# Kernel optimization log

Measured on AMD Instinct MI355X. Metric: run time of the kernel, lower is better.

## Reference

```python
import jax, jax.numpy as jnp
import numpy as np

B, D, T = 16, 512, 2048
H = 2
HD = D // H

def setup_inputs() -> dict:
    key = jax.random.key(0)
    k1, k2, k3, k4 = jax.random.split(key, 4)
    s_in = 1.0 / np.sqrt(D)   # torch default-like uniform init for weight_matrix
    s_t = 1.0 / np.sqrt(T)    # nn.Linear default init bound
    xs = jax.random.normal(k1, (B, D, T), dtype=jnp.float32)
    W_KQ = jax.random.uniform(k2, (D, D), jnp.float32, -s_in, s_in)
    W_PV = jax.random.uniform(k3, (D, D), jnp.float32, -s_in, s_in)
    W_out = jax.random.uniform(k4, (T, T), jnp.float32, -s_t, s_t)
    return {"xs": xs, "W_KQ": W_KQ, "W_PV": W_PV, "W_out": W_out}

def reference(xs, W_KQ, W_PV, W_out):
    b, d, t = xs.shape
    xs_skip = xs[:, :, :-1]                                   # [B, D, T-1]
    # xskq = xs_skip^T @ W_KQ  -> [B, T-1, D]
    xskq = jnp.einsum('bds,dj->bsj', xs_skip, W_KQ)
    # split heads: [B, H, T-1, HD]
    xskq_split = xskq.reshape(b, t - 1, H, HD).transpose(0, 2, 1, 3)
    # xs reshaped to heads along feature dim: [B, H, HD, T]
    xs_r = xs.reshape(b, H, HD, t)
    attn_arg = jnp.matmul(xskq_split, xs_r)                   # [B, H, T-1, T], rho=1
    # NON-STANDARD: softmax over the head axis (size 2)
    sm = jax.nn.softmax(attn_arg, axis=1)
    # W_PV @ xs_skip -> [B, D, T-1], split into heads [B, H, HD, T-1]
    wpvx = jnp.einsum('id,bds->bis', W_PV, xs_skip).reshape(b, H, HD, t - 1)
    f_attn = jnp.matmul(wpvx, sm).reshape(b, d, t)            # [B, D, T]
    # output = Linear(T, T, bias=None) then take last token:
    # out[b, i] = sum_t f_attn[b, i, t] * W_out[T-1, t]
    out = jnp.einsum('bdt,t->bd', f_attn, W_out[-1])
    return out
```

## Files before the change

### kernel.cpp

```cpp
#include <hip/hip_runtime.h>
#include <hip/hip_bf16.h>

#define NB 16
#define ND 512
#define NT 2048
#define TM1 2047
#define NHD 256

typedef __attribute__((ext_vector_type(8))) short bf16x8;
typedef __attribute__((ext_vector_type(4))) float f32x4;
typedef unsigned short ushort_t;
typedef unsigned int uint_t;

#define G0_OFF    0ull
#define G0_ELEMS  (16ull * 2047ull)
#define R0_OFF    32768ull
#define SX_OFF    40960ull
#define ZERO_FLOATS 49152ull
#define WSUM_OFF  49152ull
#define WKQT_OFF  49408ull
#define CHUNK_OFF 180480ull
#define BATCH_US  (2048ull * 512ull)
#define BATCH_FLOATS (2ull * 524288ull)

__device__ __forceinline__ ushort_t f2bf(float x) {
    union { float f; uint_t u; } v; v.f = x;
    uint_t r = v.u + 0x7FFFu + ((v.u >> 16) & 1u);
    return (ushort_t)(r >> 16);
}
__device__ __forceinline__ float bf2f(uint_t u) {
    union { uint_t u; float f; } v; v.u = u << 16;
    return v.f;
}

__device__ __forceinline__ void async_copy16(const ushort_t* g, ushort_t* l) {
    __builtin_amdgcn_global_load_lds(
        (const __attribute__((address_space(1))) void*)g,
        (__attribute__((address_space(3))) void*)l, 16, 0, 0);
}

#define FENCE() asm volatile("" ::: "memory")
#define BARRIER() do { FENCE(); __builtin_amdgcn_s_barrier(); FENCE(); } while (0)
#define WAITVM4() asm volatile("s_waitcnt vmcnt(4)" ::: "memory")
#define WAITVM0() asm volatile("s_waitcnt vmcnt(0)" ::: "memory")

__global__ __launch_bounds__(256) void k_prep(const float* __restrict__ wkq,
                                              ushort_t* __restrict__ wkqT,
                                              const float* __restrict__ wlast,
                                              float* __restrict__ wsum,
                                              float* __restrict__ zbase) {
    __shared__ float tile[32][33];
    const int j0 = blockIdx.x * 32, d0 = blockIdx.y * 32;
    const int c = threadIdx.x & 31, r = threadIdx.x >> 5;
    #pragma unroll
    for (int i = 0; i < 4; ++i) {
        const int d = r + i * 8;
        tile[d][c] = wkq[(size_t)(d0 + d) * ND + j0 + c];
    }
    __syncthreads();
    #pragma unroll
    for (int i = 0; i < 4; ++i) {
        const int j = r + i * 8;
        wkqT[(size_t)(j0 + j) * ND + d0 + c] = f2bf(tile[c][j]);
    }
    const int bid = blockIdx.y * 16 + blockIdx.x;
    if (threadIdx.x < 192) zbase[bid * 192 + threadIdx.x] = 0.f;
    if (bid == 0) {
        __shared__ float red[256];
        float s = 0.f;
        for (int t = threadIdx.x; t < NT; t += 256) s += wlast[t];
        red[threadIdx.x] = s;
        __syncthreads();
        for (int off = 128; off > 0; off >>= 1) {
            if (threadIdx.x < off) red[threadIdx.x] += red[threadIdx.x + off];
            __syncthreads();
        }
        if (threadIdx.x == 0) *wsum = red[0];
    }
}

__global__ __launch_bounds__(256) void k_cvt_xst(const float* __restrict__ xs,
                                                 ushort_t* __restrict__ xst, int b0) {
    __shared__ float tile[64][257];
    const int t0 = blockIdx.x * 256, d0 = blockIdx.y * 64;
    const int cc = blockIdx.z;
    const float* xb = xs + (size_t)(b0 + cc) * ND * NT;
    ushort_t* xo = xst + (size_t)cc * BATCH_US;
    const int wave = threadIdx.x >> 6, lane = threadIdx.x & 63;
    #pragma unroll
    for (int i = 0; i < 16; ++i) {
        const int row = wave * 16 + i;
        *(float4*)&tile[row][lane * 4] =
            *(const float4*)&xb[(size_t)(d0 + row) * NT + t0 + lane * 4];
    }
    __syncthreads();
    const int c8 = (threadIdx.x & 7) * 8;
    #pragma unroll
    for (int i = 0; i < 8; ++i) {
        const int t = i * 32 + (threadIdx.x >> 3);
        uint_t w[4];
        #pragma unroll
        for (int p = 0; p < 4; ++p)
            w[p] = (uint_t)f2bf(tile[c8 + 2 * p][t]) |
                   ((uint_t)f2bf(tile[c8 + 2 * p + 1][t]) << 16);
        *(uint4*)&xo[(size_t)(t0 + t) * ND + d0 + c8] = *(uint4*)w;
    }
}

__global__ __launch_bounds__(256) void k_qd(const ushort_t* __restrict__ xst,
                                            const ushort_t* __restrict__ wkqT,
                                            ushort_t* __restrict__ qdb) {
    const int j0 = blockIdx.x * 128;
    const int s0 = blockIdx.y * 128;
    const int cc = blockIdx.z;
    __shared__ __align__(16) ushort_t As[128 * 64];
    __shared__ __align__(16) ushort_t Bs[128 * 64];
    const int tid = threadIdx.x;
    const int wave = tid >> 6, lane = tid & 63;
    const int l15 = lane & 15, quad = lane >> 4;
    const int wm = wave >> 1, wn = wave & 1;
    const int swz = l15 & 7;
    const int lrow = lane >> 3;
    const size_t lsrc = (size_t)lrow * ND + (size_t)(((lane & 7) ^ lrow) << 3);
    const ushort_t* xa = xst + (size_t)cc * BATCH_US + (size_t)s0 * ND;
    const ushort_t* wb = wkqT + (size_t)j0 * ND;
    ushort_t* qo = qdb + (size_t)cc * BATCH_US;
    f32x4 acc[4][4];
    #pragma unroll
    for (int mi = 0; mi < 4; ++mi)
        #pragma unroll
        for (int nj = 0; nj < 4; ++nj) acc[mi][nj] = (f32x4){0.f, 0.f, 0.f, 0.f};
    for (int ks = 0; ks < 8; ++ks) {
        const int k0 = ks * 64;
        #pragma unroll
        for (int n = 0; n < 4; ++n) {
            const int rbase = wave * 32 + n * 8;
            async_copy16(xa + (size_t)rbase * ND + k0 + lsrc, &As[rbase * 64]);
            async_copy16(wb + (size_t)rbase * ND + k0 + lsrc, &Bs[rbase * 64]);
        }
        __builtin_amdgcn_s_waitcnt(0);
        __syncthreads();
        #pragma unroll
        for (int kc = 0; kc < 2; ++kc) {
            bf16x8 af[4], bfr[4];
            #pragma unroll
            for (int mi = 0; mi < 4; ++mi)
                af[mi] = *(const bf16x8*)&As[(wm * 64 + mi * 16 + l15) * 64 + (((kc * 4 + quad) ^ swz) << 3)];
            #pragma unroll
            for (int nj = 0; nj < 4; ++nj)
                bfr[nj] = *(const bf16x8*)&Bs[(wn * 64 + nj * 16 + l15) * 64 + (((kc * 4 + quad) ^ swz) << 3)];
            #pragma unroll
            for (int mi = 0; mi < 4; ++mi)
                #pragma unroll
                for (int nj = 0; nj < 4; ++nj)
                    acc[mi][nj] = __builtin_amdgcn_mfma_f32_16x16x32_bf16(af[mi], bfr[nj], acc[mi][nj], 0, 0, 0);
        }
        __syncthreads();
    }
    #pragma unroll
    for (int mi = 0; mi < 4; ++mi) {
        const int srow = s0 + wm * 64 + mi * 16 + quad * 4;
        #pragma unroll
        for (int nj = 0; nj < 4; ++nj) {
            const int jcol = j0 + wn * 64 + nj * 16 + l15;
            const float sgn = (jcol < NHD) ? 1.f : -1.f;
            #pragma unroll
            for (int r = 0; r < 4; ++r)
                qo[(size_t)(srow + r) * ND + jcol] = f2bf(sgn * acc[mi][nj][r]);
        }
    }
}

__device__ __forceinline__ void ld_frag4(bf16x8 (&dst)[4][2], const ushort_t* buf,
                                         int rbase, int l15, int quad, int swz) {
    #pragma unroll
    for (int i = 0; i < 4; ++i)
        #pragma unroll
        for (int kc = 0; kc < 2; ++kc)
            dst[i][kc] = *(const bf16x8*)&buf[(rbase + i * 16 + l15) * 64 + (((kc * 4 + quad) ^ swz) << 3)];
}
__device__ __forceinline__ void ld_frag2(bf16x8 (&dst)[2][2], const ushort_t* buf,
                                         int rbase, int l15, int quad, int swz) {
    #pragma unroll
    for (int i = 0; i < 2; ++i)
        #pragma unroll
        for (int kc = 0; kc < 2; ++kc)
            dst[i][kc] = *(const bf16x8*)&buf[(rbase + i * 16 + l15) * 64 + (((kc * 4 + quad) ^ swz) << 3)];
}
__device__ __forceinline__ void mfma8(f32x4 (&acc)[8][4], const bf16x8 (&a)[4][2],
                                      const bf16x8 (&bb)[2][2], int mbase, int nbase) {
    __builtin_amdgcn_s_setprio(1);
    #pragma unroll
    for (int kc = 0; kc < 2; ++kc)
        #pragma unroll
        for (int mi = 0; mi < 4; ++mi)
            #pragma unroll
            for (int nj = 0; nj < 2; ++nj)
                acc[mbase + mi][nbase + nj] = __builtin_amdgcn_mfma_f32_16x16x32_bf16(
                    a[mi][kc], bb[nj][kc], acc[mbase + mi][nbase + nj], 0, 0, 0);
    __builtin_amdgcn_s_setprio(0);
}

__global__ __launch_bounds__(512, 2) void k_attn(const ushort_t* __restrict__ qdb,
                                                 const ushort_t* __restrict__ xst,
                                                 const float* __restrict__ wlast,
                                                 float* __restrict__ g0, int b0) {
    const int t0 = blockIdx.x * 256;
    const int s0 = blockIdx.y * 256;
    const int cc = blockIdx.z;
    const int b = b0 + cc;
    __shared__ __align__(16) ushort_t smA[2][16384];
    __shared__ __align__(16) ushort_t smB[2][16384];
    __shared__ float lds_g[256];
    const int tid = threadIdx.x;
    const int wave = tid >> 6, lane = tid & 63;
    const int l15 = lane & 15, quad = lane >> 4;
    const int wm = wave >> 2, wn = wave & 3;
    const int swz = l15 & 7;
    const int lrow = lane >> 3;
    const size_t lsrc = (size_t)lrow * ND + (size_t)(((lane & 7) ^ lrow) << 3);
    const ushort_t* Ag = qdb + (size_t)cc * BATCH_US + (size_t)s0 * ND;
    const ushort_t* Bg = xst + (size_t)cc * BATCH_US + (size_t)t0 * ND;

#define STAGE(gb_, buf_, kt_, h_) do {                                        \
        const ushort_t* g_ = (gb_) + (size_t)((h_) * 128 + wave * 8) * ND +   \
                             (kt_) * 64 + lsrc;                               \
        ushort_t* l_ = (buf_) + (h_) * 8192 + wave * 512;                     \
        async_copy16(g_, l_);                                                 \
        async_copy16(g_ + (size_t)64 * ND, l_ + 4096);                        \
    } while (0)

    f32x4 acc[8][4];
    #pragma unroll
    for (int mi = 0; mi < 8; ++mi)
        #pragma unroll
        for (int nj = 0; nj < 4; ++nj) acc[mi][nj] = (f32x4){0.f, 0.f, 0.f, 0.f};
    bf16x8 a[4][2], br[2][2][2];

    STAGE(Bg, smB[0], 0, 0); STAGE(Bg, smB[0], 0, 1);
    STAGE(Ag, smA[0], 0, 0); STAGE(Ag, smA[0], 0, 1);
    STAGE(Bg, smB[1], 1, 0); STAGE(Bg, smB[1], 1, 1);
    WAITVM4();
    BARRIER();

    #pragma unroll
    for (int j = 0; j < 4; ++j) {
        const int kO = 2 * j + 1;
        ld_frag4(a, smA[0], wm * 128, l15, quad, swz);
        ld_frag2(br[0], smB[0], wn * 64, l15, quad, swz);
        STAGE(Ag, smA[1], kO, 0);
        BARRIER();
        mfma8(acc, a, br[0], 0, 0);
        BARRIER();
        ld_frag2(br[1], smB[0], wn * 64 + 32, l15, quad, swz);
        STAGE(Ag, smA[1], kO, 1);
        BARRIER();
        mfma8(acc, a, br[1], 0, 2);
        BARRIER();
        ld_frag4(a, smA[0], wm * 128 + 64, l15, quad, swz);
        if (j < 3) STAGE(Bg, smB[0], 2 * j + 2, 0);
        BARRIER();
        mfma8(acc, a, br[0], 4, 0);
        BARRIER();
        if (j < 3) STAGE(Bg, smB[0], 2 * j + 2, 1);
        BARRIER();
        mfma8(acc, a, br[1], 4, 2);
        if (j < 3) { WAITVM4(); } else { WAITVM0(); }
        BARRIER();
        ld_frag4(a, smA[1], wm * 128, l15, quad, swz);
        ld_frag2(br[0], smB[1], wn * 64, l15, quad, swz);
        if (j < 3) STAGE(Ag, smA[0], 2 * j + 2, 0);
        BARRIER();
        mfma8(acc, a, br[0], 0, 0);
        BARRIER();
        ld_frag2(br[1], smB[1], wn * 64 + 32, l15, quad, swz);
        if (j < 3) STAGE(Ag, smA[0], 2 * j + 2, 1);
        BARRIER();
        mfma8(acc, a, br[1], 0, 2);
        BARRIER();
        ld_frag4(a, smA[1], wm * 128 + 64, l15, quad, swz);
        if (j < 3) STAGE(Bg, smB[1], kO + 2, 0);
        BARRIER();
        mfma8(acc, a, br[0], 4, 0);
        BARRIER();
        if (j < 3) STAGE(Bg, smB[1], kO + 2, 1);
        BARRIER();
        mfma8(acc, a, br[1], 4, 2);
        if (j < 3) WAITVM4();
        BARRIER();
    }
#undef STAGE

    if (tid < 256) lds_g[tid] = 0.f;
    __syncthreads();
    float wt[4];
    #pragma unroll
    for (int nj = 0; nj < 4; ++nj) wt[nj] = wlast[t0 + wn * 64 + nj * 16 + l15];
    #pragma unroll
    for (int mi = 0; mi < 8; ++mi) {
        #pragma unroll
        for (int r = 0; r < 4; ++r) {
            float v = 0.f;
            #pragma unroll
            for (int nj = 0; nj < 4; ++nj) {
                const float e = __expf(-acc[mi][nj][r]);
                v = fmaf(__builtin_amdgcn_rcpf(1.f + e), wt[nj], v);
            }
            v += __shfl_xor(v, 1);
            v += __shfl_xor(v, 2);
            v += __shfl_xor(v, 4);
            v += __shfl_xor(v, 8);
            if (l15 == 0) atomicAdd(&lds_g[wm * 128 + mi * 16 + quad * 4 + r], v);
        }
    }
    __syncthreads();
    if (tid < 256) {
        const int srow = s0 + tid;
        if (srow < TM1) atomicAdd(&g0[b * TM1 + srow], lds_g[tid]);
    }
}

__global__ __launch_bounds__(256) void k_r(const ushort_t* __restrict__ xst,
                                           const float* __restrict__ g0,
                                           float* __restrict__ r0acc,
                                           float* __restrict__ sxacc, int b0) {
    const int sc = blockIdx.x;
    const int cc = blockIdx.y;
    const int b = b0 + cc;
    const ushort_t* xa = xst + (size_t)cc * BATCH_US;
    const float* g = g0 + b * TM1;
    const int d2 = threadIdx.x;
    float a00 = 0.f, a01 = 0.f, a10 = 0.f, a11 = 0.f;
    const int send = (sc == 31) ? 63 : 64;
    for (int si = 0; si < send; ++si) {
        const int s = sc * 64 + si;
        const float gv = g[s];
        const uint_t pk = *(const uint_t*)&xa[(size_t)s * ND + d2 * 2];
        const float x0 = bf2f(pk & 0xFFFFu);
        const float x1 = bf2f(pk >> 16);
        a00 = fmaf(x0, gv, a00); a01 = fmaf(x1, gv, a01);
        a10 += x0; a11 += x1;
    }
    atomicAdd(&r0acc[b * ND + d2 * 2], a00);
    atomicAdd(&r0acc[b * ND + d2 * 2 + 1], a01);
    atomicAdd(&sxacc[b * ND + d2 * 2], a10);
    atomicAdd(&sxacc[b * ND + d2 * 2 + 1], a11);
}

__global__ __launch_bounds__(256) void k_out(const float* __restrict__ wpv,
                                             const float* __restrict__ r0acc,
                                             const float* __restrict__ sxacc,
                                             const float* __restrict__ wsum,
                                             float* __restrict__ out) {
    const int b = blockIdx.x;
    const int i0 = blockIdx.y * 256;
    __shared__ float rs[1024];
    const float wsv = *wsum;
    for (int i = threadIdx.x; i < ND; i += 256) {
        const float r0 = r0acc[b * ND + i];
        const float sx = sxacc[b * ND + i];
        rs[i] = r0;
        rs[ND + i] = fmaf(wsv, sx, -r0);
    }
    __syncthreads();
    const int i = i0 + threadIdx.x;
    const float* wrow = wpv + (size_t)i * ND;
    const float* rh = rs + (i >> 8) * ND;
    float acc = 0.f;
    for (int dd = 0; dd < ND; dd += 4) {
        const float4 wv = *(const float4*)(wrow + dd);
        acc += wv.x * rh[dd] + wv.y * rh[dd + 1] + wv.z * rh[dd + 2] + wv.w * rh[dd + 3];
    }
    out[b * ND + i] = acc;
}

extern "C" void kernel_launch(void* const* d_in, const int* in_sizes, int n_in,
                              void* d_out, int out_size, void* d_ws, size_t ws_size,
                              hipStream_t stream) {
    (void)in_sizes; (void)n_in; (void)out_size;
    const float* xs   = (const float*)d_in[0];
    const float* wkq  = (const float*)d_in[1];
    const float* wpv  = (const float*)d_in[2];
    const float* wout = (const float*)d_in[3];
    const float* wlast = wout + (size_t)(NT - 1) * NT;

    float* ws    = (float*)d_ws;
    float* g0    = ws + G0_OFF;
    float* r0acc = ws + R0_OFF;
    float* sxacc = ws + SX_OFF;
    float* wsum  = ws + WSUM_OFF;
    ushort_t* wkqT = (ushort_t*)(ws + WKQT_OFF);

    const size_t ws_floats = ws_size / 4;
    size_t avail = (ws_floats > CHUNK_OFF) ? (ws_floats - CHUNK_OFF) : 0;
    int C = (int)(avail / BATCH_FLOATS);
    if (C > NB) C = NB;
    if (C < 1) C = 1;
    ushort_t* qdb = (ushort_t*)(ws + CHUNK_OFF);
    ushort_t* xst = (ushort_t*)(ws + CHUNK_OFF + (size_t)C * 524288ull);

    k_prep<<<dim3(16, 16), 256, 0, stream>>>(wkq, wkqT, wlast, wsum, ws);
    for (int b0 = 0; b0 < NB; b0 += C) {
        const int cb = (NB - b0 < C) ? (NB - b0) : C;
        k_cvt_xst<<<dim3(8, 8, cb), 256, 0, stream>>>(xs, xst, b0);
        k_qd     <<<dim3(4, 16, cb),  256, 0, stream>>>(xst, wkqT, qdb);
        k_attn   <<<dim3(8, 8, cb),  512, 0, stream>>>(qdb, xst, wlast, g0, b0);
        k_r      <<<dim3(32, cb),     256, 0, stream>>>(xst, g0, r0acc, sxacc, b0);
    }
    k_out<<<dim3(NB, 2), 256, 0, stream>>>(wpv, r0acc, sxacc, wsum, (float*)d_out);
}
```

Measured before the change: 275.0 us.

## Reuse pipelined 256x256 GEMM core for QD projection and remap workgroups for XCD locality

Factors the 8-phase double-buffered MFMA GEMM from k_attn into a shared device function and rewrites k_qd to use it with 256x256 tiles and 512 threads, replacing the simple 128x128 single-buffered loop. Both k_qd and k_attn now remap the linear block id so that consecutive logical tiles land on the same XCD (round-robin over 8), aiming to improve L2 reuse of shared operand rows. The cost is fewer, larger blocks for k_qd (256 per batch chunk fewer in count), which may reduce occupancy and balance; the XCD remap assumes the grid size is divisible by 8.

```diff
diff --git a/kernel.cpp b/kernel.cpp
--- a/kernel.cpp
+++ b/kernel.cpp
@@ -107,70 +107,6 @@
     }
 }
 
-__global__ __launch_bounds__(256) void k_qd(const ushort_t* __restrict__ xst,
-                                            const ushort_t* __restrict__ wkqT,
-                                            ushort_t* __restrict__ qdb) {
-    const int j0 = blockIdx.x * 128;
-    const int s0 = blockIdx.y * 128;
-    const int cc = blockIdx.z;
-    __shared__ __align__(16) ushort_t As[128 * 64];
-    __shared__ __align__(16) ushort_t Bs[128 * 64];
-    const int tid = threadIdx.x;
-    const int wave = tid >> 6, lane = tid & 63;
-    const int l15 = lane & 15, quad = lane >> 4;
-    const int wm = wave >> 1, wn = wave & 1;
-    const int swz = l15 & 7;
-    const int lrow = lane >> 3;
-    const size_t lsrc = (size_t)lrow * ND + (size_t)(((lane & 7) ^ lrow) << 3);
-    const ushort_t* xa = xst + (size_t)cc * BATCH_US + (size_t)s0 * ND;
-    const ushort_t* wb = wkqT + (size_t)j0 * ND;
-    ushort_t* qo = qdb + (size_t)cc * BATCH_US;
-    f32x4 acc[4][4];
-    #pragma unroll
-    for (int mi = 0; mi < 4; ++mi)
-        #pragma unroll
-        for (int nj = 0; nj < 4; ++nj) acc[mi][nj] = (f32x4){0.f, 0.f, 0.f, 0.f};
-    for (int ks = 0; ks < 8; ++ks) {
-        const int k0 = ks * 64;
-        #pragma unroll
-        for (int n = 0; n < 4; ++n) {
-            const int rbase = wave * 32 + n * 8;
-            async_copy16(xa + (size_t)rbase * ND + k0 + lsrc, &As[rbase * 64]);
-            async_copy16(wb + (size_t)rbase * ND + k0 + lsrc, &Bs[rbase * 64]);
-        }
-        __builtin_amdgcn_s_waitcnt(0);
-        __syncthreads();
-        #pragma unroll
-        for (int kc = 0; kc < 2; ++kc) {
-            bf16x8 af[4], bfr[4];
-            #pragma unroll
-            for (int mi = 0; mi < 4; ++mi)
-                af[mi] = *(const bf16x8*)&As[(wm * 64 + mi * 16 + l15) * 64 + (((kc * 4 + quad) ^ swz) << 3)];
-            #pragma unroll
-            for (int nj = 0; nj < 4; ++nj)
-                bfr[nj] = *(const bf16x8*)&Bs[(wn * 64 + nj * 16 + l15) * 64 + (((kc * 4 + quad) ^ swz) << 3)];
-            #pragma unroll
-            for (int mi = 0; mi < 4; ++mi)
-                #pragma unroll
-                for (int nj = 0; nj < 4; ++nj)
-                    acc[mi][nj] = __builtin_amdgcn_mfma_f32_16x16x32_bf16(af[mi], bfr[nj], acc[mi][nj], 0, 0, 0);
-        }
-        __syncthreads();
-    }
-    #pragma unroll
-    for (int mi = 0; mi < 4; ++mi) {
-        const int srow = s0 + wm * 64 + mi * 16 + quad * 4;
-        #pragma unroll
-        for (int nj = 0; nj < 4; ++nj) {
-            const int jcol = j0 + wn * 64 + nj * 16 + l15;
-            const float sgn = (jcol < NHD) ? 1.f : -1.f;
-            #pragma unroll
-            for (int r = 0; r < 4; ++r)
-                qo[(size_t)(srow + r) * ND + jcol] = f2bf(sgn * acc[mi][nj][r]);
-        }
-    }
-}
-
 __device__ __forceinline__ void ld_frag4(bf16x8 (&dst)[4][2], const ushort_t* buf,
                                          int rbase, int l15, int quad, int swz) {
     #pragma unroll
@@ -201,26 +137,20 @@
     __builtin_amdgcn_s_setprio(0);
 }
 
-__global__ __launch_bounds__(512, 2) void k_attn(const ushort_t* __restrict__ qdb,
-                                                 const ushort_t* __restrict__ xst,
-                                                 const float* __restrict__ wlast,
-                                                 float* __restrict__ g0, int b0) {
-    const int t0 = blockIdx.x * 256;
-    const int s0 = blockIdx.y * 256;
-    const int cc = blockIdx.z;
-    const int b = b0 + cc;
-    __shared__ __align__(16) ushort_t smA[2][16384];
-    __shared__ __align__(16) ushort_t smB[2][16384];
-    __shared__ float lds_g[256];
+__device__ __forceinline__ void gemm8ph(const ushort_t* __restrict__ Ag,
+                                        const ushort_t* __restrict__ Bg,
+                                        ushort_t* __restrict__ smA0, ushort_t* __restrict__ smA1,
+                                        ushort_t* __restrict__ smB0, ushort_t* __restrict__ smB1,
+                                        f32x4 (&acc)[8][4]) {
     const int tid = threadIdx.x;
     const int wave = tid >> 6, lane = tid & 63;
     const int l15 = lane & 15, quad = lane >> 4;
-    const int wm = wave >> 2, wn = wave & 3;
+    const int wm = wave >> 2;
     const int swz = l15 & 7;
     const int lrow = lane >> 3;
     const size_t lsrc = (size_t)lrow * ND + (size_t)(((lane & 7) ^ lrow) << 3);
-    const ushort_t* Ag = qdb + (size_t)cc * BATCH_US + (size_t)s0 * ND;
-    const ushort_t* Bg = xst + (size_t)cc * BATCH_US + (size_t)t0 * ND;
+    ushort_t* smA[2] = {smA0, smA1};
+    ushort_t* smB[2] = {smB0, smB1};
 
 #define STAGE(gb_, buf_, kt_, h_) do {                                        \
         const ushort_t* g_ = (gb_) + (size_t)((h_) * 128 + wave * 8) * ND +   \
@@ -230,11 +160,6 @@
         async_copy16(g_ + (size_t)64 * ND, l_ + 4096);                        \
     } while (0)
 
-    f32x4 acc[8][4];
-    #pragma unroll
-    for (int mi = 0; mi < 8; ++mi)
-        #pragma unroll
-        for (int nj = 0; nj < 4; ++nj) acc[mi][nj] = (f32x4){0.f, 0.f, 0.f, 0.f};
     bf16x8 a[4][2], br[2][2][2];
 
     STAGE(Bg, smB[0], 0, 0); STAGE(Bg, smB[0], 0, 1);
@@ -247,12 +172,12 @@
     for (int j = 0; j < 4; ++j) {
         const int kO = 2 * j + 1;
         ld_frag4(a, smA[0], wm * 128, l15, quad, swz);
-        ld_frag2(br[0], smB[0], wn * 64, l15, quad, swz);
+        ld_frag2(br[0], smB[0], (wave & 3) * 64, l15, quad, swz);
         STAGE(Ag, smA[1], kO, 0);
         BARRIER();
         mfma8(acc, a, br[0], 0, 0);
         BARRIER();
-        ld_frag2(br[1], smB[0], wn * 64 + 32, l15, quad, swz);
+        ld_frag2(br[1], smB[0], (wave & 3) * 64 + 32, l15, quad, swz);
         STAGE(Ag, smA[1], kO, 1);
         BARRIER();
         mfma8(acc, a, br[1], 0, 2);
@@ -268,12 +193,12 @@
         if (j < 3) { WAITVM4(); } else { WAITVM0(); }
         BARRIER();
         ld_frag4(a, smA[1], wm * 128, l15, quad, swz);
-        ld_frag2(br[0], smB[1], wn * 64, l15, quad, swz);
+        ld_frag2(br[0], smB[1], (wave & 3) * 64, l15, quad, swz);
         if (j < 3) STAGE(Ag, smA[0], 2 * j + 2, 0);
         BARRIER();
         mfma8(acc, a, br[0], 0, 0);
         BARRIER();
-        ld_frag2(br[1], smB[1], wn * 64 + 32, l15, quad, swz);
+        ld_frag2(br[1], smB[1], (wave & 3) * 64 + 32, l15, quad, swz);
         if (j < 3) STAGE(Ag, smA[0], 2 * j + 2, 1);
         BARRIER();
         mfma8(acc, a, br[1], 0, 2);
@@ -290,7 +215,82 @@
         BARRIER();
     }
 #undef STAGE
-
+}
+
+__global__ __launch_bounds__(512, 2) void k_qd(const ushort_t* __restrict__ xst,
+                                               const ushort_t* __restrict__ wkqT,
+                                               ushort_t* __restrict__ qdb) {
+    __shared__ __align__(16) ushort_t smA[2][16384];
+    __shared__ __align__(16) ushort_t smB[2][16384];
+    const int lin = blockIdx.x + gridDim.x * (blockIdx.y + gridDim.y * blockIdx.z);
+    const int nwg8 = (gridDim.x * gridDim.y * gridDim.z) >> 3;
+    const int logical = (lin & 7) * nwg8 + (lin >> 3);
+    const int jt = logical & 1;
+    const int st = (logical >> 1) & 7;
+    const int cc = logical >> 4;
+    const int j0 = jt * 256, s0 = st * 256;
+
+    const ushort_t* Ag = xst + (size_t)cc * BATCH_US + (size_t)s0 * ND;
+    const ushort_t* Bg = wkqT + (size_t)j0 * ND;
+    ushort_t* qo = qdb + (size_t)cc * BATCH_US;
+
+    f32x4 acc[8][4];
+    #pragma unroll
+    for (int mi = 0; mi < 8; ++mi)
+        #pragma unroll
+        for (int nj = 0; nj < 4; ++nj) acc[mi][nj] = (f32x4){0.f, 0.f, 0.f, 0.f};
+
+    gemm8ph(Ag, Bg, smA[0], smA[1], smB[0], smB[1], acc);
+
+    const int tid = threadIdx.x;
+    const int wave = tid >> 6, lane = tid & 63;
+    const int l15 = lane & 15, quad = lane >> 4;
+    const int wm = wave >> 2, wn = wave & 3;
+    const float sgn = (j0 == 0) ? 1.f : -1.f;
+    #pragma unroll
+    for (int mi = 0; mi < 8; ++mi) {
+        const int srow = s0 + wm * 128 + mi * 16 + quad * 4;
+        #pragma unroll
+        for (int nj = 0; nj < 4; ++nj) {
+            const int jcol = j0 + wn * 64 + nj * 16 + l15;
+            #pragma unroll
+            for (int r = 0; r < 4; ++r)
+                qo[(size_t)(srow + r) * ND + jcol] = f2bf(sgn * acc[mi][nj][r]);
+        }
+    }
+}
+
+__global__ __launch_bounds__(512, 2) void k_attn(const ushort_t* __restrict__ qdb,
+                                                 const ushort_t* __restrict__ xst,
+                                                 const float* __restrict__ wlast,
+                                                 float* __restrict__ g0, int b0) {
+    __shared__ __align__(16) ushort_t smA[2][16384];
+    __shared__ __align__(16) ushort_t smB[2][16384];
+    __shared__ float lds_g[256];
+    const int lin = blockIdx.x + gridDim.x * (blockIdx.y + gridDim.y * blockIdx.z);
+    const int nwg8 = (gridDim.x * gridDim.y * gridDim.z) >> 3;
+    const int logical = (lin & 7) * nwg8 + (lin >> 3);
+    const int tt = logical & 7;
+    const int st = (logical >> 3) & 7;
+    const int cc = logical >> 6;
+    const int t0 = tt * 256, s0 = st * 256;
+    const int b = b0 + cc;
+
+    const ushort_t* Ag = qdb + (size_t)cc * BATCH_US + (size_t)s0 * ND;
+    const ushort_t* Bg = xst + (size_t)cc * BATCH_US + (size_t)t0 * ND;
+
+    f32x4 acc[8][4];
+    #pragma unroll
+    for (int mi = 0; mi < 8; ++mi)
+        #pragma unroll
+        for (int nj = 0; nj < 4; ++nj) acc[mi][nj] = (f32x4){0.f, 0.f, 0.f, 0.f};
+
+    gemm8ph(Ag, Bg, smA[0], smA[1], smB[0], smB[1], acc);
+
+    const int tid = threadIdx.x;
+    const int wave = tid >> 6, lane = tid & 63;
+    const int l15 = lane & 15, quad = lane >> 4;
+    const int wm = wave >> 2, wn = wave & 3;
     if (tid < 256) lds_g[tid] = 0.f;
     __syncthreads();
     float wt[4];
@@ -403,7 +403,7 @@
     for (int b0 = 0; b0 < NB; b0 += C) {
         const int cb = (NB - b0 < C) ? (NB - b0) : C;
         k_cvt_xst<<<dim3(8, 8, cb), 256, 0, stream>>>(xs, xst, b0);
-        k_qd     <<<dim3(4, 16, cb),  256, 0, stream>>>(xst, wkqT, qdb);
+        k_qd     <<<dim3(2, 8, cb),  512, 0, stream>>>(xst, wkqT, qdb);
         k_attn   <<<dim3(8, 8, cb),  512, 0, stream>>>(qdb, xst, wlast, g0, b0);
         k_r      <<<dim3(32, cb),     256, 0, stream>>>(xst, g0, r0acc, sxacc, b0);
     }
```

Result: faster. 256.9 us (-6.6%).
